# Optimization experiments

Hardware: AMD Instinct MI355X
Metric: run time of the kernel (lower is better)

The kernel has to match this reference:

```python
import jax, jax.numpy as jnp
import numpy as np

N, T, F = 20000, 64, 128          # nodes, time steps, feat_dim
B, K = 8192, 32                   # queries, padded neighbor count
WWIN = 64                         # window_w -> delta table size WWIN+1
DD, MD, HD, HH = 16, 64, 128, 64  # delta_dim, msg_dim, hidden_dim, h_dim
Q = 3 * B                         # (v,s,z) x B node-time aggregations


def _lin(k, i, o):
    k1, k2 = jax.random.split(k)
    w = jax.random.normal(k1, (i, o), jnp.float32) / np.sqrt(i).astype(np.float32)
    b = jax.random.normal(k2, (o,), jnp.float32) * 0.01
    return w, b


def setup_inputs() -> dict:
    key = jax.random.key(0)
    ks = jax.random.split(key, 24)
    x_tensor = jax.random.normal(ks[0], (N, T, F), jnp.float32)
    node_ids = jax.random.randint(ks[1], (Q,), 0, N)
    times = jax.random.randint(ks[2], (Q,), 0, T)
    in_u = jax.random.randint(ks[3], (Q, K), 0, N)
    in_tau = jax.random.randint(ks[4], (Q, K), 0, T)
    in_mask = jax.random.uniform(ks[5], (Q, K)) < 0.5
    out_u = jax.random.randint(ks[6], (Q, K), 0, N)
    out_tau = jax.random.randint(ks[7], (Q, K), 0, T)
    out_mask = jax.random.uniform(ks[8], (Q, K)) < 0.5
    d_norm = jax.random.uniform(ks[9], (B,))
    delta_emb = jax.random.normal(ks[10], (WWIN + 1, DD), jnp.float32) * 0.1
    piw1, pib1 = _lin(ks[11], F + DD, MD)
    piw2, pib2 = _lin(ks[12], MD, MD)
    pow1, pob1 = _lin(ks[13], F + DD, MD)
    pow2, pob2 = _lin(ks[14], MD, MD)
    cw1, cb1 = _lin(ks[15], F + 2 * MD, HD)
    cw2, cb2 = _lin(ks[16], HD, HH)
    sw1, sb1 = _lin(ks[17], 3 * HH + 1, HD)
    sw2, sb2 = _lin(ks[18], HD, 1)
    return dict(x_tensor=x_tensor, d_norm=d_norm, delta_emb=delta_emb,
                piw1=piw1, pib1=pib1, piw2=piw2, pib2=pib2,
                pow1=pow1, pob1=pob1, pow2=pow2, pob2=pob2,
                cw1=cw1, cb1=cb1, cw2=cw2, cb2=cb2,
                sw1=sw1, sb1=sb1, sw2=sw2, sb2=sb2,
                node_ids=node_ids, times=times,
                in_u=in_u, in_tau=in_tau, in_mask=in_mask,
                out_u=out_u, out_tau=out_tau, out_mask=out_mask)


def reference(x_tensor, d_norm, delta_emb,
              piw1, pib1, piw2, pib2,
              pow1, pob1, pow2, pob2,
              cw1, cb1, cw2, cb2,
              sw1, sb1, sw2, sb2,
              node_ids, times, in_u, in_tau, in_mask, out_u, out_tau, out_mask):
    def mlp2(x, w1, b1, w2, b2):  # Linear -> ReLU -> Linear
        return jnp.maximum(x @ w1 + b1, 0.0) @ w2 + b2

    def agg(u, tau, mask, sign, w1, b1, w2, b2):
        # sign=+1: in arcs delta = clamp(t - tau); sign=-1: out arcs delta = clamp(tau - t)
        delta = jnp.clip(sign * (times[:, None] - tau), 0, WWIN)     # [Q,K]
        x_u = x_tensor[u, tau]                                        # [Q,K,F] gather
        msg = mlp2(jnp.concatenate([x_u, delta_emb[delta]], -1), w1, b1, w2, b2)  # [Q,K,MD]
        m = mask[..., None].astype(msg.dtype)
        return (msg * m).sum(1) / jnp.maximum(m.sum(1), 1.0)         # masked mean; empty -> zeros

    m_in = agg(in_u, in_tau, in_mask, 1, piw1, pib1, piw2, pib2)
    m_out = agg(out_u, out_tau, out_mask, -1, pow1, pob1, pow2, pob2)
    x_vt = x_tensor[node_ids, times]                                  # [Q,F]
    # combine: Linear -> ReLU -> (Dropout eval) -> Linear -> ReLU
    h = jnp.maximum(mlp2(jnp.concatenate([x_vt, m_in, m_out], -1), cw1, cb1, cw2, cb2), 0.0)  # [Q,HH]
    feat = jnp.concatenate([h.reshape(B, 3 * HH), d_norm[:, None]], -1)  # [B, 3*HH+1]
    return mlp2(feat, sw1, sb1, sw2, sb2)[:, 0]                       # [B]
```

## Files before the change

### kernel.cpp

```cpp
#include <hip/hip_runtime.h>
#include <hip/hip_bf16.h>

#define NND   20000
#define TSTEP 64
#define FF    128
#define BB    8192
#define KK    32
#define QQ    (3*BB)
#define WWINC 64
#define DDIM  16
#define MDIM  64
#define HDIM  128
#define HHDIM 64

typedef __attribute__((ext_vector_type(8)))  short short8;
typedef __attribute__((ext_vector_type(16))) float f32x16;

union FragU { unsigned u[4]; short8 s; };

static __device__ __forceinline__ unsigned pkbf(float a, float b) {
    union { float f; unsigned u; } ua, ub; ua.f = a; ub.f = b;
    unsigned ra = (ua.u + 0x7FFFu + ((ua.u >> 16) & 1u)) >> 16;
    unsigned rb = (ub.u + 0x7FFFu + ((ub.u >> 16) & 1u)) >> 16;
    return (ra & 0xFFFFu) | (rb << 16);
}
static __device__ __forceinline__ unsigned short f2bf(float a) {
    union { float f; unsigned u; } v; v.f = a;
    return (unsigned short)((v.u + 0x7FFFu + ((v.u >> 16) & 1u)) >> 16);
}

#define NW  4
#define HLD 72

__global__ __launch_bounds__(256, 3)
void agg_mfma_kernel(const float* __restrict__ x, const float* __restrict__ demb,
                     const float* __restrict__ w1, const float* __restrict__ b1,
                     const float* __restrict__ w2, const float* __restrict__ b2,
                     const int* __restrict__ times, const int* __restrict__ uu,
                     const int* __restrict__ tt, const int* __restrict__ mm,
                     float* __restrict__ mout, const int sign, const int nwaves)
{
    __shared__ short w1f[9 * 2 * 64 * 8];
    __shared__ short Hs[NW][KK * HLD];

    const int tid  = threadIdx.x;
    const int lane = tid & 63;
    const int wv   = tid >> 6;
    const int r    = lane & 31;
    const int hi   = lane >> 5;

    for (int f = tid; f < 9 * 2 * 64; f += 256) {
        const int ln = f & 63, sn = f >> 6, s = sn >> 1, n = sn & 1;
        const int krow = 16 * s + 8 * (ln >> 5);
        const int col  = 32 * n + (ln & 31);
        #pragma unroll
        for (int i = 0; i < 8; i += 2) {
            const float va = w1[(krow + i) * MDIM + col];
            const float vb = w1[(krow + i + 1) * MDIM + col];
            *(unsigned*)&w1f[f * 8 + i] = pkbf(va, vb);
        }
    }
    short8 w2f[4][2];
    #pragma unroll
    for (int s = 0; s < 4; s++)
        #pragma unroll
        for (int n = 0; n < 2; n++) {
            FragU fu;
            #pragma unroll
            for (int i = 0; i < 8; i += 2) {
                const float va = w2[(16 * s + 8 * hi + i) * MDIM + 32 * n + r];
                const float vb = w2[(16 * s + 8 * hi + i + 1) * MDIM + 32 * n + r];
                fu.u[i >> 1] = pkbf(va, vb);
            }
            w2f[s][n] = fu.s;
        }
    const float b1c0 = b1[r], b1c1 = b1[32 + r];
    const float b2c0 = b2[r], b2c1 = b2[32 + r];
    __syncthreads();

    const int gwave = blockIdx.x * NW + wv;
    for (int q = gwave; q < QQ; q += nwaves) {
        const int t = times[q];
        int xb = 0, db = 0, mk = 0;
        if (lane < KK) {
            const int u   = uu[q * KK + lane];
            const int tau = tt[q * KK + lane];
            mk = mm[q * KK + lane];
            int d = (sign > 0) ? (t - tau) : (tau - t);
            d = d < 0 ? 0 : (d > WWINC ? WWINC : d);
            xb = u * (TSTEP * FF) + tau * FF;
            db = d * DDIM;
        }
        const unsigned long long bal = __ballot(mk != 0);
        const float cnt  = (float)__popcll(bal);
        const float cinv = 1.0f / fmaxf(cnt, 1.0f);
        const float has  = cnt > 0.0f ? 1.0f : 0.0f;
        const int xbr = __shfl(xb, r, 64);
        const int dbr = __shfl(db, r, 64);
        const int mkr = __shfl(mk, r, 64);

        f32x16 acc0, acc1;
        #pragma unroll
        for (int i = 0; i < 16; i++) { acc0[i] = 0.0f; acc1[i] = 0.0f; }

        const float* xrow = x + xbr + 8 * hi;
        #pragma unroll 4
        for (int s = 0; s < 8; s++) {
            float4 p0 = make_float4(0.f, 0.f, 0.f, 0.f), p1 = p0;
            if (mkr) {
                p0 = *(const float4*)(xrow + 16 * s);
                p1 = *(const float4*)(xrow + 16 * s + 4);
            }
            FragU fa;
            fa.u[0] = pkbf(p0.x, p0.y); fa.u[1] = pkbf(p0.z, p0.w);
            fa.u[2] = pkbf(p1.x, p1.y); fa.u[3] = pkbf(p1.z, p1.w);
            const short8 bf0 = *(const short8*)&w1f[(s * 2 + 0) * 512 + lane * 8];
            const short8 bf1 = *(const short8*)&w1f[(s * 2 + 1) * 512 + lane * 8];
            acc0 = __builtin_amdgcn_mfma_f32_32x32x16_bf16(fa.s, bf0, acc0, 0, 0, 0);
            acc1 = __builtin_amdgcn_mfma_f32_32x32x16_bf16(fa.s, bf1, acc1, 0, 0, 0);
        }
        {
            float4 p0 = make_float4(0.f, 0.f, 0.f, 0.f), p1 = p0;
            if (mkr) {
                p0 = *(const float4*)(demb + dbr + 8 * hi);
                p1 = *(const float4*)(demb + dbr + 8 * hi + 4);
            }
            FragU fa;
            fa.u[0] = pkbf(p0.x, p0.y); fa.u[1] = pkbf(p0.z, p0.w);
            fa.u[2] = pkbf(p1.x, p1.y); fa.u[3] = pkbf(p1.z, p1.w);
            const short8 bf0 = *(const short8*)&w1f[(8 * 2 + 0) * 512 + lane * 8];
            const short8 bf1 = *(const short8*)&w1f[(8 * 2 + 1) * 512 + lane * 8];
            acc0 = __builtin_amdgcn_mfma_f32_32x32x16_bf16(fa.s, bf0, acc0, 0, 0, 0);
            acc1 = __builtin_amdgcn_mfma_f32_32x32x16_bf16(fa.s, bf1, acc1, 0, 0, 0);
        }

        #pragma unroll
        for (int g = 0; g < 16; g++) {
            const int rr = (g & 3) + 8 * (g >> 2) + 4 * hi;
            const float mrow = (float)((bal >> rr) & 1ull);
            const float h0 = fmaxf(acc0[g] + b1c0, 0.0f) * mrow;
            const float h1 = fmaxf(acc1[g] + b1c1, 0.0f) * mrow;
            Hs[wv][rr * HLD + r]      = (short)f2bf(h0);
            Hs[wv][rr * HLD + 32 + r] = (short)f2bf(h1);
        }

        f32x16 c0, c1;
        #pragma unroll
        for (int i = 0; i < 16; i++) { c0[i] = 0.0f; c1[i] = 0.0f; }
        #pragma unroll
        for (int s = 0; s < 4; s++) {
            const short8 a = *(const short8*)&Hs[wv][r * HLD + 16 * s + 8 * hi];
            c0 = __builtin_amdgcn_mfma_f32_32x32x16_bf16(a, w2f[s][0], c0, 0, 0, 0);
            c1 = __builtin_amdgcn_mfma_f32_32x32x16_bf16(a, w2f[s][1], c1, 0, 0, 0);
        }

        float p0s = 0.0f, p1s = 0.0f;
        #pragma unroll
        for (int g = 0; g < 16; g++) { p0s += c0[g]; p1s += c1[g]; }
        p0s += __shfl_xor(p0s, 32, 64);
        p1s += __shfl_xor(p1s, 32, 64);
        const float outv = (hi ? p1s : p0s) * cinv + (hi ? b2c1 : b2c0) * has;
        mout[(size_t)q * MDIM + 32 * hi + r] = outv;
    }
}

#define G2 16
#define FEATP 260
#define H1P   132

#define FMA8(cc, base) do { \
    const float4 wa_ = *(const float4*)(base); \
    const float4 wb_ = *(const float4*)((base) + 4); \
    acc[0] = fmaf((cc), wa_.x, acc[0]); acc[1] = fmaf((cc), wa_.y, acc[1]); \
    acc[2] = fmaf((cc), wa_.z, acc[2]); acc[3] = fmaf((cc), wa_.w, acc[3]); \
    acc[4] = fmaf((cc), wb_.x, acc[4]); acc[5] = fmaf((cc), wb_.y, acc[5]); \
    acc[6] = fmaf((cc), wb_.z, acc[6]); acc[7] = fmaf((cc), wb_.w, acc[7]); \
  } while (0)

__global__ __launch_bounds__(256, 2)
void combine_kernel(const float* __restrict__ x,
                    const float* __restrict__ cw1, const float* __restrict__ cb1,
                    const float* __restrict__ cw2, const float* __restrict__ cb2,
                    const int* __restrict__ node_ids, const int* __restrict__ times,
                    const float* __restrict__ min_ws, const float* __restrict__ mout_ws,
                    float* __restrict__ h_ws)
{
    __shared__ float feat[G2 * FEATP];
    __shared__ float h1b[G2 * H1P];
    __shared__ float cw2s[HDIM * HHDIM];
    __shared__ float cb1s[HDIM];
    __shared__ float cb2s[HHDIM];
    __shared__ int   xb[G2];

    const int tid = threadIdx.x;
    for (int i = tid; i < HDIM * HHDIM; i += 256) cw2s[i] = cw2[i];
    if (tid < HDIM)  cb1s[tid] = cb1[tid];
    if (tid < HHDIM) cb2s[tid] = cb2[tid];
    __syncthreads();

    const int g = tid >> 4;
    const int j = tid & 15;

    for (int qb = blockIdx.x * G2; qb < QQ; qb += gridDim.x * G2) {
        if (tid < G2) xb[tid] = node_ids[qb + tid] * (TSTEP * FF) + times[qb + tid] * FF;
        __syncthreads();
        for (int e = tid; e < G2 * 64; e += 256) {
            const int gg = e >> 6, c = e & 63;
            const int q = qb + gg;
            float4 v;
            if (c < 32)      v = *(const float4*)(x + xb[gg] + c * 4);
            else if (c < 48) v = *(const float4*)(min_ws  + (size_t)q * MDIM + (c - 32) * 4);
            else             v = *(const float4*)(mout_ws + (size_t)q * MDIM + (c - 48) * 4);
            *(float4*)(feat + gg * FEATP + c * 4) = v;
        }
        __syncthreads();

        float acc[8];
        {
            const float* fr = feat + g * FEATP;
            #pragma unroll
            for (int r2 = 0; r2 < 8; r2++) acc[r2] = cb1s[j * 8 + r2];
            #pragma unroll 4
            for (int i = 0; i < 2 * HDIM; i++) {
                const float f = fr[i];
                FMA8(f, cw1 + i * HDIM + j * 8);
            }
            #pragma unroll
            for (int r2 = 0; r2 < 8; r2++) acc[r2] = fmaxf(acc[r2], 0.0f);
        }
        *(float4*)(h1b + g * H1P + j * 8)     = make_float4(acc[0], acc[1], acc[2], acc[3]);
        *(float4*)(h1b + g * H1P + j * 8 + 4) = make_float4(acc[4], acc[5], acc[6], acc[7]);
        __syncthreads();

        {
            float a2[4];
            #pragma unroll
            for (int r2 = 0; r2 < 4; r2++) a2[r2] = cb2s[j * 4 + r2];
            const float* hr = h1b + g * H1P;
            #pragma unroll 4
            for (int i = 0; i < HDIM; i++) {
                const float hh = hr[i];
                const float4 w = *(const float4*)(cw2s + i * HHDIM + j * 4);
                a2[0] = fmaf(hh, w.x, a2[0]); a2[1] = fmaf(hh, w.y, a2[1]);
                a2[2] = fmaf(hh, w.z, a2[2]); a2[3] = fmaf(hh, w.w, a2[3]);
            }
            #pragma unroll
            for (int r2 = 0; r2 < 4; r2++) a2[r2] = fmaxf(a2[r2], 0.0f);
            *(float4*)(h_ws + (size_t)(qb + g) * HHDIM + j * 4) =
                make_float4(a2[0], a2[1], a2[2], a2[3]);
        }
        __syncthreads();
    }
}

#define G3 8
#define SFP 200

__global__ __launch_bounds__(256, 2)
void score_kernel(const float* __restrict__ h_ws, const float* __restrict__ dnorm,
                  const float* __restrict__ sw1, const float* __restrict__ sb1,
                  const float* __restrict__ sw2, const float* __restrict__ sb2,
                  float* __restrict__ out)
{
    __shared__ float featb[G3 * SFP];
    __shared__ float sw2s[HDIM];
    __shared__ float sb1s[HDIM];

    const int tid = threadIdx.x;
    if (tid < HDIM) { sw2s[tid] = sw2[tid]; sb1s[tid] = sb1[tid]; }
    __syncthreads();

    const int g = tid >> 5;
    const int j = tid & 31;

    for (int bb = blockIdx.x * G3; bb < BB; bb += gridDim.x * G3) {
        for (int e = tid; e < G3 * 48; e += 256) {
            const int gg = e / 48, c = e - gg * 48;
            *(float4*)(featb + gg * SFP + c * 4) =
                *(const float4*)(h_ws + (size_t)(bb + gg) * 192 + c * 4);
        }
        if (tid < G3) featb[tid * SFP + 192] = dnorm[bb + tid];
        __syncthreads();

        float a[4];
        #pragma unroll
        for (int r2 = 0; r2 < 4; r2++) a[r2] = sb1s[j * 4 + r2];
        const float* fr = featb + g * SFP;
        for (int i = 0; i < 193; i++) {
            const float f = fr[i];
            const float4 w = *(const float4*)(sw1 + i * HDIM + j * 4);
            a[0] = fmaf(f, w.x, a[0]); a[1] = fmaf(f, w.y, a[1]);
            a[2] = fmaf(f, w.z, a[2]); a[3] = fmaf(f, w.w, a[3]);
        }
        float p = 0.0f;
        #pragma unroll
        for (int r2 = 0; r2 < 4; r2++) p += fmaxf(a[r2], 0.0f) * sw2s[j * 4 + r2];
        for (int off = 16; off > 0; off >>= 1) p += __shfl_down(p, off, 32);
        if (j == 0) out[bb + g] = p + sb2[0];
        __syncthreads();
    }
}

extern "C" void kernel_launch(void* const* d_in, const int* in_sizes, int n_in,
                              void* d_out, int out_size, void* d_ws, size_t ws_size,
                              hipStream_t stream)
{
    const float* x     = (const float*)d_in[0];
    const float* dnorm = (const float*)d_in[1];
    const float* demb  = (const float*)d_in[2];
    const float* piw1  = (const float*)d_in[3];
    const float* pib1  = (const float*)d_in[4];
    const float* piw2  = (const float*)d_in[5];
    const float* pib2  = (const float*)d_in[6];
    const float* pow1  = (const float*)d_in[7];
    const float* pob1  = (const float*)d_in[8];
    const float* pow2  = (const float*)d_in[9];
    const float* pob2  = (const float*)d_in[10];
    const float* cw1   = (const float*)d_in[11];
    const float* cb1   = (const float*)d_in[12];
    const float* cw2   = (const float*)d_in[13];
    const float* cb2   = (const float*)d_in[14];
    const float* sw1   = (const float*)d_in[15];
    const float* sb1   = (const float*)d_in[16];
    const float* sw2   = (const float*)d_in[17];
    const float* sb2   = (const float*)d_in[18];
    const int* node_ids = (const int*)d_in[19];
    const int* times    = (const int*)d_in[20];
    const int* in_u     = (const int*)d_in[21];
    const int* in_tau   = (const int*)d_in[22];
    const int* in_mask  = (const int*)d_in[23];
    const int* out_u    = (const int*)d_in[24];
    const int* out_tau  = (const int*)d_in[25];
    const int* out_mask = (const int*)d_in[26];

    float* ws      = (float*)d_ws;
    float* min_ws  = ws;
    float* mout_ws = ws + (size_t)QQ * MDIM;
    float* h_ws    = ws + (size_t)2 * QQ * MDIM;
    float* out     = (float*)d_out;

    const int grid = 768;
    const int nwaves = grid * NW;

    agg_mfma_kernel<<<grid, 256, 0, stream>>>(x, demb, piw1, pib1, piw2, pib2,
                                              times, in_u, in_tau, in_mask,
                                              min_ws, 1, nwaves);
    agg_mfma_kernel<<<grid, 256, 0, stream>>>(x, demb, pow1, pob1, pow2, pob2,
                                              times, out_u, out_tau, out_mask,
                                              mout_ws, -1, nwaves);
    combine_kernel<<<512, 256, 0, stream>>>(x, cw1, cb1, cw2, cb2,
                                            node_ids, times, min_ws, mout_ws, h_ws);
    score_kernel<<<256, 256, 0, stream>>>(h_ws, dnorm, sw1, sb1, sw2, sb2, out);
}
```

Before: 1.028 ms.

## Move combine and score MLPs onto bf16 MFMA with pre-packed weight fragments

Replaces the scalar-FMA combine and score kernels with single-wave MFMA kernels that process 32 rows per block. A new pack kernel converts cw1, cw2 and sw1 to bf16 in MFMA fragment order each call, and the combine hidden output is now stored as bf16. The aim is to cut the FP32 FMA cost of these two stages. In exchange, precision drops to bf16 for those layers, and there is an extra kernel launch.

After: 919.1 us. 1.12x faster.

```diff
diff --git a/kernel.cpp b/kernel.cpp
--- a/kernel.cpp
+++ b/kernel.cpp
@@ -24,9 +24,44 @@
     unsigned rb = (ub.u + 0x7FFFu + ((ub.u >> 16) & 1u)) >> 16;
     return (ra & 0xFFFFu) | (rb << 16);
 }
-static __device__ __forceinline__ unsigned short f2bf(float a) {
+static __device__ __forceinline__ short f2bf(float a) {
     union { float f; unsigned u; } v; v.f = a;
-    return (unsigned short)((v.u + 0x7FFFu + ((v.u >> 16) & 1u)) >> 16);
+    return (short)((v.u + 0x7FFFu + ((v.u >> 16) & 1u)) >> 16);
+}
+
+__global__ void pack_kernel(const float* __restrict__ cw1, const float* __restrict__ cw2,
+                            const float* __restrict__ sw1,
+                            short* __restrict__ cw1f, short* __restrict__ cw2f,
+                            short* __restrict__ sw1f)
+{
+    const int gid = blockIdx.x * 256 + threadIdx.x;
+    const int ln  = gid & 63;
+    const int f   = gid >> 6;
+    const int kr8 = 8 * (ln >> 5);
+    const int c   = ln & 31;
+    FragU v;
+    if (f < 64) {
+        const int s = f >> 2, n = f & 3;
+        #pragma unroll
+        for (int i = 0; i < 8; i += 2)
+            v.u[i >> 1] = pkbf(cw1[(16*s + kr8 + i)     * HDIM + 32*n + c],
+                               cw1[(16*s + kr8 + i + 1) * HDIM + 32*n + c]);
+        *(short8*)&cw1f[f * 512 + ln * 8] = v.s;
+    } else if (f < 80) {
+        const int f2 = f - 64, s = f2 >> 1, n = f2 & 1;
+        #pragma unroll
+        for (int i = 0; i < 8; i += 2)
+            v.u[i >> 1] = pkbf(cw2[(16*s + kr8 + i)     * HHDIM + 32*n + c],
+                               cw2[(16*s + kr8 + i + 1) * HHDIM + 32*n + c]);
+        *(short8*)&cw2f[f2 * 512 + ln * 8] = v.s;
+    } else {
+        const int f3 = f - 80, s = f3 >> 2, n = f3 & 3;
+        #pragma unroll
+        for (int i = 0; i < 8; i += 2)
+            v.u[i >> 1] = pkbf(sw1[(16*s + kr8 + i)     * HDIM + 32*n + c],
+                               sw1[(16*s + kr8 + i + 1) * HDIM + 32*n + c]);
+        *(short8*)&sw1f[f3 * 512 + ln * 8] = v.s;
+    }
 }
 
 #define NW  4
@@ -140,8 +175,8 @@
             const float mrow = (float)((bal >> rr) & 1ull);
             const float h0 = fmaxf(acc0[g] + b1c0, 0.0f) * mrow;
             const float h1 = fmaxf(acc1[g] + b1c1, 0.0f) * mrow;
-            Hs[wv][rr * HLD + r]      = (short)f2bf(h0);
-            Hs[wv][rr * HLD + 32 + r] = (short)f2bf(h1);
+            Hs[wv][rr * HLD + r]      = f2bf(h0);
+            Hs[wv][rr * HLD + 32 + r] = f2bf(h1);
         }
 
         f32x16 c0, c1;
@@ -164,140 +199,150 @@
     }
 }
 
-#define G2 16
-#define FEATP 260
-#define H1P   132
-
-#define FMA8(cc, base) do { \
-    const float4 wa_ = *(const float4*)(base); \
-    const float4 wb_ = *(const float4*)((base) + 4); \
-    acc[0] = fmaf((cc), wa_.x, acc[0]); acc[1] = fmaf((cc), wa_.y, acc[1]); \
-    acc[2] = fmaf((cc), wa_.z, acc[2]); acc[3] = fmaf((cc), wa_.w, acc[3]); \
-    acc[4] = fmaf((cc), wb_.x, acc[4]); acc[5] = fmaf((cc), wb_.y, acc[5]); \
-    acc[6] = fmaf((cc), wb_.z, acc[6]); acc[7] = fmaf((cc), wb_.w, acc[7]); \
-  } while (0)
-
-__global__ __launch_bounds__(256, 2)
-void combine_kernel(const float* __restrict__ x,
-                    const float* __restrict__ cw1, const float* __restrict__ cb1,
-                    const float* __restrict__ cw2, const float* __restrict__ cb2,
-                    const int* __restrict__ node_ids, const int* __restrict__ times,
-                    const float* __restrict__ min_ws, const float* __restrict__ mout_ws,
-                    float* __restrict__ h_ws)
+#define HLD2 136
+
+__global__ __launch_bounds__(64, 2)
+void combine_mfma(const float* __restrict__ x,
+                  const int* __restrict__ node_ids, const int* __restrict__ times,
+                  const float* __restrict__ min_ws, const float* __restrict__ mout_ws,
+                  const short* __restrict__ cw1f, const float* __restrict__ cb1,
+                  const short* __restrict__ cw2f, const float* __restrict__ cb2,
+                  short* __restrict__ h_bf)
 {
-    __shared__ float feat[G2 * FEATP];
-    __shared__ float h1b[G2 * H1P];
-    __shared__ float cw2s[HDIM * HHDIM];
-    __shared__ float cb1s[HDIM];
-    __shared__ float cb2s[HHDIM];
-    __shared__ int   xb[G2];
-
-    const int tid = threadIdx.x;
-    for (int i = tid; i < HDIM * HHDIM; i += 256) cw2s[i] = cw2[i];
-    if (tid < HDIM)  cb1s[tid] = cb1[tid];
-    if (tid < HHDIM) cb2s[tid] = cb2[tid];
+    __shared__ short Hs[KK * HLD2];
+    const int lane = threadIdx.x & 63;
+    const int r = lane & 31, hi = lane >> 5;
+    const int qb = blockIdx.x * 32;
+    const int q  = qb + r;
+    const int xb = node_ids[q] * (TSTEP * FF) + times[q] * FF;
+
+    f32x16 acc[4];
+    #pragma unroll
+    for (int n = 0; n < 4; n++)
+        #pragma unroll
+        for (int i = 0; i < 16; i++) acc[n][i] = 0.0f;
+
+    const float* xrow = x + xb + 8 * hi;
+    #pragma unroll
+    for (int s = 0; s < 8; s++) {
+        const float4 p0 = *(const float4*)(xrow + 16 * s);
+        const float4 p1 = *(const float4*)(xrow + 16 * s + 4);
+        FragU fa;
+        fa.u[0] = pkbf(p0.x, p0.y); fa.u[1] = pkbf(p0.z, p0.w);
+        fa.u[2] = pkbf(p1.x, p1.y); fa.u[3] = pkbf(p1.z, p1.w);
+        #pragma unroll
+        for (int n = 0; n < 4; n++) {
+            const short8 bf = *(const short8*)&cw1f[(s * 4 + n) * 512 + lane * 8];
+            acc[n] = __builtin_amdgcn_mfma_f32_32x32x16_bf16(fa.s, bf, acc[n], 0, 0, 0);
+        }
+    }
+    const float* mrow = min_ws + (size_t)q * MDIM + 8 * hi;
+    #pragma unroll
+    for (int s = 0; s < 4; s++) {
+        const float4 p0 = *(const float4*)(mrow + 16 * s);
+        const float4 p1 = *(const float4*)(mrow + 16 * s + 4);
+        FragU fa;
+        fa.u[0] = pkbf(p0.x, p0.y); fa.u[1] = pkbf(p0.z, p0.w);
+        fa.u[2] = pkbf(p1.x, p1.y); fa.u[3] = pkbf(p1.z, p1.w);
+        #pragma unroll
+        for (int n = 0; n < 4; n++) {
+            const short8 bf = *(const short8*)&cw1f[((s + 8) * 4 + n) * 512 + lane * 8];
+            acc[n] = __builtin_amdgcn_mfma_f32_32x32x16_bf16(fa.s, bf, acc[n], 0, 0, 0);
+        }
+    }
+    const float* orow = mout_ws + (size_t)q * MDIM + 8 * hi;
+    #pragma unroll
+    for (int s = 0; s < 4; s++) {
+        const float4 p0 = *(const float4*)(orow + 16 * s);
+        const float4 p1 = *(const float4*)(orow + 16 * s + 4);
+        FragU fa;
+        fa.u[0] = pkbf(p0.x, p0.y); fa.u[1] = pkbf(p0.z, p0.w);
+        fa.u[2] = pkbf(p1.x, p1.y); fa.u[3] = pkbf(p1.z, p1.w);
+        #pragma unroll
+        for (int n = 0; n < 4; n++) {
+            const short8 bf = *(const short8*)&cw1f[((s + 12) * 4 + n) * 512 + lane * 8];
+            acc[n] = __builtin_amdgcn_mfma_f32_32x32x16_bf16(fa.s, bf, acc[n], 0, 0, 0);
+        }
+    }
+
+    #pragma unroll
+    for (int n = 0; n < 4; n++) {
+        const float bias = cb1[32 * n + r];
+        #pragma unroll
+        for (int g = 0; g < 16; g++) {
+            const int rr = (g & 3) + 8 * (g >> 2) + 4 * hi;
+            Hs[rr * HLD2 + 32 * n + r] = f2bf(fmaxf(acc[n][g] + bias, 0.0f));
+        }
+    }
     __syncthreads();
 
-    const int g = tid >> 4;
-    const int j = tid & 15;
-
-    for (int qb = blockIdx.x * G2; qb < QQ; qb += gridDim.x * G2) {
-        if (tid < G2) xb[tid] = node_ids[qb + tid] * (TSTEP * FF) + times[qb + tid] * FF;
-        __syncthreads();
-        for (int e = tid; e < G2 * 64; e += 256) {
-            const int gg = e >> 6, c = e & 63;
-            const int q = qb + gg;
-            float4 v;
-            if (c < 32)      v = *(const float4*)(x + xb[gg] + c * 4);
-            else if (c < 48) v = *(const float4*)(min_ws  + (size_t)q * MDIM + (c - 32) * 4);
-            else             v = *(const float4*)(mout_ws + (size_t)q * MDIM + (c - 48) * 4);
-            *(float4*)(feat + gg * FEATP + c * 4) = v;
-        }
-        __syncthreads();
-
-        float acc[8];
-        {
-            const float* fr = feat + g * FEATP;
-            #pragma unroll
-            for (int r2 = 0; r2 < 8; r2++) acc[r2] = cb1s[j * 8 + r2];
-            #pragma unroll 4
-            for (int i = 0; i < 2 * HDIM; i++) {
-                const float f = fr[i];
-                FMA8(f, cw1 + i * HDIM + j * 8);
-            }
-            #pragma unroll
-            for (int r2 = 0; r2 < 8; r2++) acc[r2] = fmaxf(acc[r2], 0.0f);
-        }
-        *(float4*)(h1b + g * H1P + j * 8)     = make_float4(acc[0], acc[1], acc[2], acc[3]);
-        *(float4*)(h1b + g * H1P + j * 8 + 4) = make_float4(acc[4], acc[5], acc[6], acc[7]);
-        __syncthreads();
-
-        {
-            float a2[4];
-            #pragma unroll
-            for (int r2 = 0; r2 < 4; r2++) a2[r2] = cb2s[j * 4 + r2];
-            const float* hr = h1b + g * H1P;
-            #pragma unroll 4
-            for (int i = 0; i < HDIM; i++) {
-                const float hh = hr[i];
-                const float4 w = *(const float4*)(cw2s + i * HHDIM + j * 4);
-                a2[0] = fmaf(hh, w.x, a2[0]); a2[1] = fmaf(hh, w.y, a2[1]);
-                a2[2] = fmaf(hh, w.z, a2[2]); a2[3] = fmaf(hh, w.w, a2[3]);
-            }
-            #pragma unroll
-            for (int r2 = 0; r2 < 4; r2++) a2[r2] = fmaxf(a2[r2], 0.0f);
-            *(float4*)(h_ws + (size_t)(qb + g) * HHDIM + j * 4) =
-                make_float4(a2[0], a2[1], a2[2], a2[3]);
-        }
-        __syncthreads();
-    }
-}
-
-#define G3 8
-#define SFP 200
-
-__global__ __launch_bounds__(256, 2)
-void score_kernel(const float* __restrict__ h_ws, const float* __restrict__ dnorm,
-                  const float* __restrict__ sw1, const float* __restrict__ sb1,
-                  const float* __restrict__ sw2, const float* __restrict__ sb2,
-                  float* __restrict__ out)
+    f32x16 c0, c1;
+    #pragma unroll
+    for (int i = 0; i < 16; i++) { c0[i] = 0.0f; c1[i] = 0.0f; }
+    #pragma unroll
+    for (int s = 0; s < 8; s++) {
+        const short8 a = *(const short8*)&Hs[r * HLD2 + 16 * s + 8 * hi];
+        const short8 b0 = *(const short8*)&cw2f[(s * 2 + 0) * 512 + lane * 8];
+        const short8 b1v = *(const short8*)&cw2f[(s * 2 + 1) * 512 + lane * 8];
+        c0 = __builtin_amdgcn_mfma_f32_32x32x16_bf16(a, b0, c0, 0, 0, 0);
+        c1 = __builtin_amdgcn_mfma_f32_32x32x16_bf16(a, b1v, c1, 0, 0, 0);
+    }
+    const float bb0 = cb2[r], bb1 = cb2[32 + r];
+    #pragma unroll
+    for (int g = 0; g < 16; g++) {
+        const int rr = (g & 3) + 8 * (g >> 2) + 4 * hi;
+        h_bf[(size_t)(qb + rr) * HHDIM + r]      = f2bf(fmaxf(c0[g] + bb0, 0.0f));
+        h_bf[(size_t)(qb + rr) * HHDIM + 32 + r] = f2bf(fmaxf(c1[g] + bb1, 0.0f));
+    }
+}
+
+__global__ __launch_bounds__(64, 2)
+void score_mfma(const short* __restrict__ h_bf, const float* __restrict__ dnorm,
+                const short* __restrict__ sw1f, const float* __restrict__ sw1,
+                const float* __restrict__ sb1, const float* __restrict__ sw2,
+                const float* __restrict__ sb2, float* __restrict__ out)
 {
-    __shared__ float featb[G3 * SFP];
-    __shared__ float sw2s[HDIM];
-    __shared__ float sb1s[HDIM];
-
-    const int tid = threadIdx.x;
-    if (tid < HDIM) { sw2s[tid] = sw2[tid]; sb1s[tid] = sb1[tid]; }
-    __syncthreads();
-
-    const int g = tid >> 5;
-    const int j = tid & 31;
-
-    for (int bb = blockIdx.x * G3; bb < BB; bb += gridDim.x * G3) {
-        for (int e = tid; e < G3 * 48; e += 256) {
-            const int gg = e / 48, c = e - gg * 48;
-            *(float4*)(featb + gg * SFP + c * 4) =
-                *(const float4*)(h_ws + (size_t)(bb + gg) * 192 + c * 4);
-        }
-        if (tid < G3) featb[tid * SFP + 192] = dnorm[bb + tid];
-        __syncthreads();
-
-        float a[4];
-        #pragma unroll
-        for (int r2 = 0; r2 < 4; r2++) a[r2] = sb1s[j * 4 + r2];
-        const float* fr = featb + g * SFP;
-        for (int i = 0; i < 193; i++) {
-            const float f = fr[i];
-            const float4 w = *(const float4*)(sw1 + i * HDIM + j * 4);
-            a[0] = fmaf(f, w.x, a[0]); a[1] = fmaf(f, w.y, a[1]);
-            a[2] = fmaf(f, w.z, a[2]); a[3] = fmaf(f, w.w, a[3]);
-        }
+    const int lane = threadIdx.x & 63;
+    const int r = lane & 31, hi = lane >> 5;
+    const int bb = blockIdx.x * 32;
+
+    f32x16 acc[4];
+    #pragma unroll
+    for (int n = 0; n < 4; n++)
+        #pragma unroll
+        for (int i = 0; i < 16; i++) acc[n][i] = 0.0f;
+
+    const short* arow = h_bf + (size_t)(bb + r) * 192 + 8 * hi;
+    #pragma unroll
+    for (int s = 0; s < 12; s++) {
+        const short8 a = *(const short8*)(arow + 16 * s);
+        #pragma unroll
+        for (int n = 0; n < 4; n++) {
+            const short8 bf = *(const short8*)&sw1f[(s * 4 + n) * 512 + lane * 8];
+            acc[n] = __builtin_amdgcn_mfma_f32_32x32x16_bf16(a, bf, acc[n], 0, 0, 0);
+        }
+    }
+
+    float sb1c[4], swr[4], sw2c[4];
+    #pragma unroll
+    for (int n = 0; n < 4; n++) {
+        sb1c[n] = sb1[32 * n + r];
+        swr[n]  = sw1[192 * HDIM + 32 * n + r];
+        sw2c[n] = sw2[32 * n + r];
+    }
+    const float sb2v = sb2[0];
+
+    #pragma unroll
+    for (int g = 0; g < 16; g++) {
+        const int rr = (g & 3) + 8 * (g >> 2) + 4 * hi;
+        const float dn = dnorm[bb + rr];
         float p = 0.0f;
         #pragma unroll
-        for (int r2 = 0; r2 < 4; r2++) p += fmaxf(a[r2], 0.0f) * sw2s[j * 4 + r2];
-        for (int off = 16; off > 0; off >>= 1) p += __shfl_down(p, off, 32);
-        if (j == 0) out[bb + g] = p + sb2[0];
-        __syncthreads();
+        for (int n = 0; n < 4; n++)
+            p += fmaxf(acc[n][g] + sb1c[n] + dn * swr[n], 0.0f) * sw2c[n];
+        p += __shfl_xor(p, 1);  p += __shfl_xor(p, 2);  p += __shfl_xor(p, 4);
+        p += __shfl_xor(p, 8);  p += __shfl_xor(p, 16);
+        if (r == 0) out[bb + rr] = p + sb2v;
     }
 }
 
@@ -336,19 +381,24 @@
     float* ws      = (float*)d_ws;
     float* min_ws  = ws;
     float* mout_ws = ws + (size_t)QQ * MDIM;
-    float* h_ws    = ws + (size_t)2 * QQ * MDIM;
+    short* h_bf    = (short*)(ws + (size_t)2 * QQ * MDIM);
+    short* wpack   = (short*)(ws + (size_t)2 * QQ * MDIM + (size_t)BB * 192 / 2);
+    short* cw1f    = wpack;
+    short* cw2f    = wpack + 32768;
+    short* sw1f    = wpack + 40960;
     float* out     = (float*)d_out;
 
     const int grid = 768;
     const int nwaves = grid * NW;
 
+    pack_kernel<<<32, 256, 0, stream>>>(cw1, cw2, sw1, cw1f, cw2f, sw1f);
     agg_mfma_kernel<<<grid, 256, 0, stream>>>(x, demb, piw1, pib1, piw2, pib2,
                                               times, in_u, in_tau, in_mask,
                                               min_ws, 1, nwaves);
     agg_mfma_kernel<<<grid, 256, 0, stream>>>(x, demb, pow1, pob1, pow2, pob2,
                                               times, out_u, out_tau, out_mask,
                                               mout_ws, -1, nwaves);
-    combine_kernel<<<512, 256, 0, stream>>>(x, cw1, cb1, cw2, cb2,
-                                            node_ids, times, min_ws, mout_ws, h_ws);
-    score_kernel<<<256, 256, 0, stream>>>(h_ws, dnorm, sw1, sb1, sw2, sb2, out);
-}
+    combine_mfma<<<QQ / 32, 64, 0, stream>>>(x, node_ids, times, min_ws, mout_ws,
+                                             cw1f, cb1, cw2f, cb2, h_bf);
+    score_mfma<<<BB / 32, 64, 0, stream>>>(h_bf, dnorm, sw1f, sw1, sb1, sw2, sb2, out);
+}
```
